# Kernel optimization log

Measured on AMD Instinct MI355X. Metric: run time of the kernel, lower is better.

## Reference

```python
import jax, jax.numpy as jnp
import numpy as np

B, D_IMG, D_NUM, P = 16384, 2048, 256, 128

def setup_inputs() -> dict:
    key = jax.random.key(0)
    ks = jax.random.split(key, 12)
    s = lambda d: 1.0 / np.sqrt(d)
    return {
        "img_feat": jax.random.normal(ks[0], (B, D_IMG), jnp.float32),
        "num_feat": jax.random.normal(ks[1], (B, D_NUM), jnp.float32),
        "Wi1": jax.random.uniform(ks[2], (D_IMG, P), jnp.float32, -s(D_IMG), s(D_IMG)),
        "bi1": jax.random.uniform(ks[3], (P,), jnp.float32, -s(D_IMG), s(D_IMG)),
        "Wi2": jax.random.uniform(ks[4], (P, P), jnp.float32, -s(P), s(P)),
        "bi2": jax.random.uniform(ks[5], (P,), jnp.float32, -s(P), s(P)),
        "Wn1": jax.random.uniform(ks[6], (D_NUM, P), jnp.float32, -s(D_NUM), s(D_NUM)),
        "bn1": jax.random.uniform(ks[7], (P,), jnp.float32, -s(D_NUM), s(D_NUM)),
        "Wn2": jax.random.uniform(ks[8], (P, P), jnp.float32, -s(P), s(P)),
        "bn2": jax.random.uniform(ks[9], (P,), jnp.float32, -s(P), s(P)),
        "log_temp": jnp.asarray(np.log(0.1), jnp.float32),
    }

def _mlp(x, W1, b1, W2, b2):
    h = jax.nn.relu(x @ W1 + b1)
    return h @ W2 + b2

def _l2norm(x, eps=1e-12):
    # matches F.normalize(dim=1): x / max(||x||, eps)
    n = jnp.sqrt(jnp.sum(x * x, axis=1, keepdims=True))
    return x / jnp.maximum(n, eps)

def reference(img_feat, num_feat, Wi1, bi1, Wi2, bi2, Wn1, bn1, Wn2, bn2, log_temp):
    temp = jnp.exp(log_temp)
    ip = _l2norm(_mlp(img_feat, Wi1, bi1, Wi2, bi2))  # [B, P]
    npj = _l2norm(_mlp(num_feat, Wn1, bn1, Wn2, bn2))  # [B, P]
    logits = (ip @ npj.T) / temp                        # [B, B]
    # symmetric cross-entropy with labels = arange(B): targets on the diagonal
    lse_rows = jax.nn.logsumexp(logits, axis=1)  # i2n
    lse_cols = jax.nn.logsumexp(logits, axis=0)  # n2i (logits.T rows)
    diag = jnp.diagonal(logits)
    loss_i2n = jnp.mean(lse_rows - diag)
    loss_n2i = jnp.mean(lse_cols - diag)
    return (loss_i2n + loss_n2i) * 0.5
```

## Files before the change

kernel.cpp:

```cpp
#include <hip/hip_runtime.h>
#include <hip/hip_bf16.h>

typedef __bf16 bf16_t;
typedef __bf16 bf16x8 __attribute__((ext_vector_type(8)));
typedef float f32x4 __attribute__((ext_vector_type(4)));

#define NB 16384
#define NSPLIT 16
#define CG (NB / NSPLIT)
#define BNT 64
#define NT (CG / BNT)

__device__ inline bf16x8 ld8(const bf16_t* p) { return *(const bf16x8*)p; }

__device__ inline void gload_lds16(const bf16_t* g, bf16_t* l) {
  __builtin_amdgcn_global_load_lds(
      (const __attribute__((address_space(1))) unsigned int*)g,
      (__attribute__((address_space(3))) unsigned int*)l, 16, 0, 0);
}

__global__ void prep(const float* __restrict__ Wi1, const float* __restrict__ Wn1,
                     const float* __restrict__ Wi2, const float* __restrict__ Wn2,
                     bf16_t* __restrict__ Wi1t, bf16_t* __restrict__ Wn1t,
                     bf16_t* __restrict__ Wi2t, bf16_t* __restrict__ Wn2t,
                     float* __restrict__ lossacc) {
  int b = blockIdx.x;
  if (b < 1280) {
    int idx = b * 256 + threadIdx.x;
    if (idx < 262144) { int k = idx >> 7, n = idx & 127;
      Wi1t[n * 2048 + (k ^ ((n & 7) << 3))] = (bf16_t)Wi1[idx]; return; }
    idx -= 262144;
    if (idx < 32768) { int k = idx >> 7, n = idx & 127;
      Wn1t[n * 256 + (k ^ ((n & 7) << 3))] = (bf16_t)Wn1[idx]; return; }
    idx -= 32768;
    if (idx < 16384) { int k = idx >> 7, n = idx & 127;
      Wi2t[n * 128 + (k ^ ((n & 7) << 3))] = (bf16_t)Wi2[idx]; return; }
    idx -= 16384;
    { int k = idx >> 7, n = idx & 127;
      Wn2t[n * 128 + (k ^ ((n & 7) << 3))] = (bf16_t)Wn2[idx]; }
  } else {
    if (threadIdx.x < 2) lossacc[threadIdx.x] = 0.f;
  }
}

__global__ __launch_bounds__(256, 2) void mlp_fused(
    const float* __restrict__ imgf, const float* __restrict__ numf,
    const bf16_t* __restrict__ Wi1t, const bf16_t* __restrict__ Wn1t,
    const bf16_t* __restrict__ Wi2t, const bf16_t* __restrict__ Wn2t,
    const float* __restrict__ bi1, const float* __restrict__ bn1,
    const float* __restrict__ bi2, const float* __restrict__ bn2,
    bf16_t* __restrict__ ipb, bf16_t* __restrict__ npb) {
  __shared__ bf16_t As[2][32 * 128];
  __shared__ bf16_t Bs[2][128 * 128];
  const int bid = blockIdx.x;
  const bool isnum = bid >= 512;
  const float*  Xf = isnum ? numf : imgf;
  const bf16_t* W1 = isnum ? Wn1t : Wi1t;
  const bf16_t* W2 = isnum ? Wn2t : Wi2t;
  const float* b1  = isnum ? bn1 : bi1;
  const float* b2  = isnum ? bn2 : bi2;
  bf16_t* Out = isnum ? npb : ipb;
  const int K = isnum ? 256 : 2048;
  const int NK = K >> 7;
  const int t = threadIdx.x, l = t & 63, wid = t >> 6;
  const int wm = wid >> 1, wn = wid & 1;
  const int row0 = (bid & 511) * 32;

  auto stageA = [&](int kk, int buf) {
#pragma unroll
    for (int i = 0; i < 2; i++) {
      int s = t + i * 256;
      int r = s >> 4, c = s & 15;
      const float* src = Xf + (size_t)(row0 + r) * K + kk * 128 + c * 8;
      float4 f0 = *(const float4*)(src);
      float4 f1 = *(const float4*)(src + 4);
      bf16x8 v;
      v[0]=(bf16_t)f0.x; v[1]=(bf16_t)f0.y; v[2]=(bf16_t)f0.z; v[3]=(bf16_t)f0.w;
      v[4]=(bf16_t)f1.x; v[5]=(bf16_t)f1.y; v[6]=(bf16_t)f1.z; v[7]=(bf16_t)f1.w;
      *(bf16x8*)(As[buf] + r * 128 + ((c ^ (r & 7)) << 3)) = v;
    }
  };
  auto stageB = [&](int kk, int buf) {
#pragma unroll
    for (int i = 0; i < 8; i++) {
      int s = t + i * 256;
      gload_lds16(W1 + (size_t)(s >> 4) * K + kk * 128 + (s & 15) * 8,
                  Bs[buf] + s * 8);
    }
  };

  f32x4 acc[4];
#pragma unroll
  for (int j = 0; j < 4; j++) acc[j] = (f32x4){0.f, 0.f, 0.f, 0.f};

  stageA(0, 0);
  stageB(0, 0);
  __syncthreads();

  for (int kk = 0; kk < NK; kk++) {
    const int cur = kk & 1;
    if (kk + 1 < NK) {
      stageA(kk + 1, cur ^ 1);
      stageB(kk + 1, cur ^ 1);
    }
#pragma unroll
    for (int ks = 0; ks < 4; ks++) {
      int r = wm * 16 + (l & 15);
      int c = ks * 4 + (l >> 4);
      bf16x8 a = ld8(As[cur] + r * 128 + ((c ^ (r & 7)) << 3));
#pragma unroll
      for (int nt = 0; nt < 4; nt++) {
        int rb = wn * 64 + nt * 16 + (l & 15);
        bf16x8 bfr = ld8(Bs[cur] + rb * 128 + ((c ^ (rb & 7)) << 3));
        acc[nt] = __builtin_amdgcn_mfma_f32_16x16x32_bf16(a, bfr, acc[nt], 0, 0, 0);
      }
    }
    __syncthreads();
  }

  float* rnorm = (float*)As[1];
#pragma unroll
  for (int i = 0; i < 8; i++) {
    int s = t + i * 256;
    gload_lds16(W2 + (size_t)(s >> 4) * 128 + (s & 15) * 8, Bs[0] + s * 8);
  }
  if (t < 32) rnorm[t] = 0.f;
  {
    int rbase = wm * 16 + ((l >> 4) << 2);
#pragma unroll
    for (int nt = 0; nt < 4; nt++) {
      int col = wn * 64 + nt * 16 + (l & 15);
      float bv = b1[col];
#pragma unroll
      for (int r4 = 0; r4 < 4; r4++) {
        int row = rbase + r4;
        float h = fmaxf(acc[nt][r4] + bv, 0.f);
        As[0][row * 128 + (col ^ ((row & 7) << 3))] = (bf16_t)h;
      }
    }
  }
  __syncthreads();

  f32x4 acc2[4];
#pragma unroll
  for (int j = 0; j < 4; j++) acc2[j] = (f32x4){0.f, 0.f, 0.f, 0.f};
#pragma unroll
  for (int ks = 0; ks < 4; ks++) {
    int r = wm * 16 + (l & 15);
    int c = ks * 4 + (l >> 4);
    bf16x8 a = ld8(As[0] + r * 128 + ((c ^ (r & 7)) << 3));
#pragma unroll
    for (int nt = 0; nt < 4; nt++) {
      int rb = wn * 64 + nt * 16 + (l & 15);
      bf16x8 bfr = ld8(Bs[0] + rb * 128 + ((c ^ (rb & 7)) << 3));
      acc2[nt] = __builtin_amdgcn_mfma_f32_16x16x32_bf16(a, bfr, acc2[nt], 0, 0, 0);
    }
  }
  float vv[4][4];
#pragma unroll
  for (int nt = 0; nt < 4; nt++) {
    int col = wn * 64 + nt * 16 + (l & 15);
    float bv = b2[col];
#pragma unroll
    for (int r4 = 0; r4 < 4; r4++) vv[nt][r4] = acc2[nt][r4] + bv;
  }
#pragma unroll
  for (int r4 = 0; r4 < 4; r4++) {
    float p = 0.f;
#pragma unroll
    for (int nt = 0; nt < 4; nt++) p += vv[nt][r4] * vv[nt][r4];
    p += __shfl_xor(p, 1); p += __shfl_xor(p, 2);
    p += __shfl_xor(p, 4); p += __shfl_xor(p, 8);
    if ((l & 15) == 0) atomicAdd(&rnorm[wm * 16 + ((l >> 4) << 2) + r4], p);
  }
  __syncthreads();
#pragma unroll
  for (int r4 = 0; r4 < 4; r4++) {
    int rl = wm * 16 + ((l >> 4) << 2) + r4;
    float sc = 1.f / fmaxf(sqrtf(rnorm[rl]), 1e-12f);
#pragma unroll
    for (int nt = 0; nt < 4; nt++) {
      int col = wn * 64 + nt * 16 + (l & 15);
      int swcol = col ^ ((rl & 7) << 3);
      Out[(size_t)(row0 + rl) * 128 + swcol] = (bf16_t)(vv[nt][r4] * sc);
    }
  }
}

__global__ __launch_bounds__(512, 4) void logits_split(
    const bf16_t* __restrict__ IP, const bf16_t* __restrict__ NP,
    const float* __restrict__ log_temp, float* __restrict__ rowpart,
    float* __restrict__ colpart, float* __restrict__ diag) {
  __shared__ bf16_t BsAll[2 * BNT * 128];
  __shared__ float colred[CG];
  __shared__ float rowred[2][128];
  int bid = blockIdx.x;
  int sw = (bid & 7) * (128 * NSPLIT / 8) + (bid >> 3);
  int bm = sw >> 4, g = sw & (NSPLIT - 1);
  const int t = threadIdx.x, l = t & 63, wid = t >> 6;
  const int wm = wid >> 1, wn = wid & 1;
  const float invt = __expf(-log_temp[0]);
  const float kk = invt * 1.44269504088896f;

  for (int i = t; i < CG; i += 512) colred[i] = 0.f;
#pragma unroll
  for (int i = 0; i < 4; i++) {
    int s = t + i * 512;
    gload_lds16(IP + (size_t)bm * (128 * 128) + s * 8, BsAll + s * 8);
  }
  __syncthreads();
  bf16x8 af[2][4];
#pragma unroll
  for (int mt = 0; mt < 2; mt++) {
    int r = wm * 32 + mt * 16 + (l & 15);
#pragma unroll
    for (int ks = 0; ks < 4; ks++) {
      int c = ks * 4 + (l >> 4);
      af[mt][ks] = ld8(BsAll + r * 128 + ((c ^ (r & 7)) << 3));
    }
  }
  __syncthreads();
#pragma unroll
  for (int i = 0; i < 2; i++) {
    int s = t + i * 512;
    gload_lds16(NP + (size_t)(g * CG) * 128 + s * 8, BsAll + s * 8);
  }
  __syncthreads();

  f32x4 racc[2];
  racc[0] = (f32x4){0.f, 0.f, 0.f, 0.f};
  racc[1] = (f32x4){0.f, 0.f, 0.f, 0.f};

#pragma unroll 1
  for (int tl = 0; tl < NT; tl++) {
    bf16_t* Bsc = BsAll + (tl & 1) * (BNT * 128);
    if (tl + 1 < NT) {
      bf16_t* Bsn = BsAll + ((tl + 1) & 1) * (BNT * 128);
      const bf16_t* src = NP + (size_t)(g * CG + (tl + 1) * BNT) * 128;
#pragma unroll
      for (int i = 0; i < 2; i++) {
        int s = t + i * 512;
        gload_lds16(src + s * 8, Bsn + s * 8);
      }
    }
    f32x4 acc[2][2];
#pragma unroll
    for (int i = 0; i < 2; i++)
#pragma unroll
      for (int j = 0; j < 2; j++) acc[i][j] = (f32x4){0.f, 0.f, 0.f, 0.f};
#pragma unroll
    for (int ks = 0; ks < 4; ks++) {
      int c = ks * 4 + (l >> 4);
      bf16x8 b[2];
#pragma unroll
      for (int nt = 0; nt < 2; nt++) {
        int rb = wn * 32 + nt * 16 + (l & 15);
        b[nt] = ld8(Bsc + rb * 128 + ((c ^ (rb & 7)) << 3));
      }
#pragma unroll
      for (int mt = 0; mt < 2; mt++) {
        acc[mt][0] = __builtin_amdgcn_mfma_f32_16x16x32_bf16(af[mt][ks], b[0], acc[mt][0], 0, 0, 0);
        acc[mt][1] = __builtin_amdgcn_mfma_f32_16x16x32_bf16(af[mt][ks], b[1], acc[mt][1], 0, 0, 0);
      }
    }
    const int colbase = g * CG + tl * BNT;
    if ((colbase >> 7) == bm) {
#pragma unroll
      for (int mt = 0; mt < 2; mt++)
#pragma unroll
        for (int nt = 0; nt < 2; nt++)
#pragma unroll
          for (int r4 = 0; r4 < 4; r4++) {
            int gr = bm * 128 + wm * 32 + mt * 16 + ((l >> 4) << 2) + r4;
            int gc = colbase + wn * 32 + nt * 16 + (l & 15);
            if (gr == gc) diag[gr] = acc[mt][nt][r4] * invt;
          }
    }
#pragma unroll
    for (int mt = 0; mt < 2; mt++)
#pragma unroll
      for (int nt = 0; nt < 2; nt++) {
        f32x4 y = acc[mt][nt] * kk - kk;
#pragma unroll
        for (int r4 = 0; r4 < 4; r4++) acc[mt][nt][r4] = __builtin_amdgcn_exp2f(y[r4]);
      }
#pragma unroll
    for (int mt = 0; mt < 2; mt++) racc[mt] += acc[mt][0] + acc[mt][1];
#pragma unroll
    for (int nt = 0; nt < 2; nt++) {
      f32x4 cv = acc[0][nt] + acc[1][nt];
      float cs = (cv[0] + cv[1]) + (cv[2] + cv[3]);
      cs += __shfl_xor(cs, 16); cs += __shfl_xor(cs, 32);
      if (l < 16) atomicAdd(&colred[tl * BNT + wn * 32 + nt * 16 + l], cs);
    }
    __syncthreads();
  }
#pragma unroll
  for (int mt = 0; mt < 2; mt++)
#pragma unroll
    for (int r4 = 0; r4 < 4; r4++) {
      float rs = racc[mt][r4];
      rs += __shfl_xor(rs, 1); rs += __shfl_xor(rs, 2);
      rs += __shfl_xor(rs, 4); rs += __shfl_xor(rs, 8);
      if ((l & 15) == 0)
        rowred[wn][wm * 32 + mt * 16 + ((l >> 4) << 2) + r4] = rs;
    }
  __syncthreads();
  if (t < 128)
    rowpart[(size_t)g * NB + bm * 128 + t] = rowred[0][t] + rowred[1][t];
  for (int c = t; c < CG; c += 512)
    colpart[(size_t)bm * NB + g * CG + c] = colred[c];
}

__global__ void finalize(const float* __restrict__ rowpart, const float* __restrict__ colpart,
                         const float* __restrict__ diag, const float* __restrict__ log_temp,
                         float* __restrict__ lossacc, float* __restrict__ out) {
  int i = blockIdx.x * 64 + threadIdx.x;
  float rsum = 0.f, csum = 0.f;
#pragma unroll
  for (int g = 0; g < NSPLIT; g++) rsum += rowpart[(size_t)g * NB + i];
#pragma unroll 16
  for (int b = 0; b < 128; b++) csum += colpart[(size_t)b * NB + i];
  float v = 0.5f * (logf(rsum) + logf(csum)) - diag[i];
  for (int m = 1; m < 64; m <<= 1) v += __shfl_xor(v, m);
  if (threadIdx.x == 0) {
    atomicAdd(lossacc, v);
    __threadfence();
    unsigned n = atomicAdd((unsigned*)(lossacc + 1), 1u);
    if (n == gridDim.x - 1) {
      float tot = atomicAdd(lossacc, 0.f);
      out[0] = tot / (float)NB + __expf(-log_temp[0]);
    }
  }
}

extern "C" void kernel_launch(void* const* d_in, const int* in_sizes, int n_in,
                              void* d_out, int out_size, void* d_ws, size_t ws_size,
                              hipStream_t stream) {
  const float* img = (const float*)d_in[0];
  const float* num = (const float*)d_in[1];
  const float* Wi1 = (const float*)d_in[2];
  const float* bi1 = (const float*)d_in[3];
  const float* Wi2 = (const float*)d_in[4];
  const float* bi2 = (const float*)d_in[5];
  const float* Wn1 = (const float*)d_in[6];
  const float* bn1 = (const float*)d_in[7];
  const float* Wn2 = (const float*)d_in[8];
  const float* bn2 = (const float*)d_in[9];
  const float* log_temp = (const float*)d_in[10];
  float* out = (float*)d_out;

  char* w = (char*)d_ws;
  bf16_t* ipb  = (bf16_t*)(w);
  bf16_t* npb  = (bf16_t*)(w + (4u << 20));
  float* colpart = (float*)(w + (8u << 20));
  bf16_t* Wi1t = (bf16_t*)(w + (16u << 20));
  bf16_t* Wn1t = (bf16_t*)(w + (16u << 20) + (512u << 10));
  bf16_t* Wi2t = (bf16_t*)(w + (16u << 20) + (576u << 10));
  bf16_t* Wn2t = (bf16_t*)(w + (16u << 20) + (640u << 10));
  float* rowpart = (float*)(w + (16u << 20));
  float* diag    = (float*)(w + (17u << 20));
  float* lossacc = (float*)(w + (17u << 20) + (64u << 10));

  prep<<<dim3(1281), 256, 0, stream>>>(Wi1, Wn1, Wi2, Wn2,
                                       Wi1t, Wn1t, Wi2t, Wn2t, lossacc);
  mlp_fused<<<dim3(1024), 256, 0, stream>>>(img, num, Wi1t, Wn1t, Wi2t, Wn2t,
                                            bi1, bn1, bi2, bn2, ipb, npb);
  logits_split<<<dim3(128 * NSPLIT), 512, 0, stream>>>(ipb, npb, log_temp,
                                                       rowpart, colpart, diag);
  finalize<<<dim3(NB / 64), 64, 0, stream>>>(rowpart, colpart, diag, log_temp,
                                             lossacc, out);
}
```

Measured before the change: 356.5 us.

## Split MLP launch per path, enlarge logits warp tiles, split finalize reduction

The fused MLP kernel is split into two launches, one for the image path and one for the numeric path, so each branch is specialized and K is passed in. The logits kernel moves from 512 to 256 threads per block, so each warp computes 64 rows instead of 32 and reuses every loaded B fragment across four MFMA row tiles, at the cost of more registers and an occupancy bound of 3. The finalize step is split into a wide column-sum kernel and a separate loss kernel to parallelize the 128-way column reduction better. This adds one extra launch and an intermediate buffer.

```diff
diff --git a/kernel.cpp b/kernel.cpp
--- a/kernel.cpp
+++ b/kernel.cpp
@@ -43,28 +43,16 @@
   }
 }
 
-__global__ __launch_bounds__(256, 2) void mlp_fused(
-    const float* __restrict__ imgf, const float* __restrict__ numf,
-    const bf16_t* __restrict__ Wi1t, const bf16_t* __restrict__ Wn1t,
-    const bf16_t* __restrict__ Wi2t, const bf16_t* __restrict__ Wn2t,
-    const float* __restrict__ bi1, const float* __restrict__ bn1,
-    const float* __restrict__ bi2, const float* __restrict__ bn2,
-    bf16_t* __restrict__ ipb, bf16_t* __restrict__ npb) {
+__global__ __launch_bounds__(256, 2) void mlp_path(
+    const float* __restrict__ Xf, const bf16_t* __restrict__ W1,
+    const bf16_t* __restrict__ W2, const float* __restrict__ b1,
+    const float* __restrict__ b2, bf16_t* __restrict__ Out, int K) {
   __shared__ bf16_t As[2][32 * 128];
   __shared__ bf16_t Bs[2][128 * 128];
-  const int bid = blockIdx.x;
-  const bool isnum = bid >= 512;
-  const float*  Xf = isnum ? numf : imgf;
-  const bf16_t* W1 = isnum ? Wn1t : Wi1t;
-  const bf16_t* W2 = isnum ? Wn2t : Wi2t;
-  const float* b1  = isnum ? bn1 : bi1;
-  const float* b2  = isnum ? bn2 : bi2;
-  bf16_t* Out = isnum ? npb : ipb;
-  const int K = isnum ? 256 : 2048;
   const int NK = K >> 7;
   const int t = threadIdx.x, l = t & 63, wid = t >> 6;
   const int wm = wid >> 1, wn = wid & 1;
-  const int row0 = (bid & 511) * 32;
+  const int row0 = blockIdx.x * 32;
 
   auto stageA = [&](int kk, int buf) {
 #pragma unroll
@@ -187,7 +175,7 @@
   }
 }
 
-__global__ __launch_bounds__(512, 4) void logits_split(
+__global__ __launch_bounds__(256, 3) void logits_split(
     const bf16_t* __restrict__ IP, const bf16_t* __restrict__ NP,
     const float* __restrict__ log_temp, float* __restrict__ rowpart,
     float* __restrict__ colpart, float* __restrict__ diag) {
@@ -202,17 +190,17 @@
   const float invt = __expf(-log_temp[0]);
   const float kk = invt * 1.44269504088896f;
 
-  for (int i = t; i < CG; i += 512) colred[i] = 0.f;
-#pragma unroll
-  for (int i = 0; i < 4; i++) {
-    int s = t + i * 512;
+  for (int i = t; i < CG; i += 256) colred[i] = 0.f;
+#pragma unroll
+  for (int i = 0; i < 8; i++) {
+    int s = t + i * 256;
     gload_lds16(IP + (size_t)bm * (128 * 128) + s * 8, BsAll + s * 8);
   }
   __syncthreads();
-  bf16x8 af[2][4];
-#pragma unroll
-  for (int mt = 0; mt < 2; mt++) {
-    int r = wm * 32 + mt * 16 + (l & 15);
+  bf16x8 af[4][4];
+#pragma unroll
+  for (int mt = 0; mt < 4; mt++) {
+    int r = wm * 64 + mt * 16 + (l & 15);
 #pragma unroll
     for (int ks = 0; ks < 4; ks++) {
       int c = ks * 4 + (l >> 4);
@@ -221,15 +209,15 @@
   }
   __syncthreads();
 #pragma unroll
-  for (int i = 0; i < 2; i++) {
-    int s = t + i * 512;
+  for (int i = 0; i < 4; i++) {
+    int s = t + i * 256;
     gload_lds16(NP + (size_t)(g * CG) * 128 + s * 8, BsAll + s * 8);
   }
   __syncthreads();
 
-  f32x4 racc[2];
-  racc[0] = (f32x4){0.f, 0.f, 0.f, 0.f};
-  racc[1] = (f32x4){0.f, 0.f, 0.f, 0.f};
+  f32x4 racc[4];
+#pragma unroll
+  for (int a = 0; a < 4; a++) racc[a] = (f32x4){0.f, 0.f, 0.f, 0.f};
 
 #pragma unroll 1
   for (int tl = 0; tl < NT; tl++) {
@@ -238,14 +226,14 @@
       bf16_t* Bsn = BsAll + ((tl + 1) & 1) * (BNT * 128);
       const bf16_t* src = NP + (size_t)(g * CG + (tl + 1) * BNT) * 128;
 #pragma unroll
-      for (int i = 0; i < 2; i++) {
-        int s = t + i * 512;
+      for (int i = 0; i < 4; i++) {
+        int s = t + i * 256;
         gload_lds16(src + s * 8, Bsn + s * 8);
       }
     }
-    f32x4 acc[2][2];
-#pragma unroll
-    for (int i = 0; i < 2; i++)
+    f32x4 acc[4][2];
+#pragma unroll
+    for (int i = 0; i < 4; i++)
 #pragma unroll
       for (int j = 0; j < 2; j++) acc[i][j] = (f32x4){0.f, 0.f, 0.f, 0.f};
 #pragma unroll
@@ -258,7 +246,7 @@
         b[nt] = ld8(Bsc + rb * 128 + ((c ^ (rb & 7)) << 3));
       }
 #pragma unroll
-      for (int mt = 0; mt < 2; mt++) {
+      for (int mt = 0; mt < 4; mt++) {
         acc[mt][0] = __builtin_amdgcn_mfma_f32_16x16x32_bf16(af[mt][ks], b[0], acc[mt][0], 0, 0, 0);
         acc[mt][1] = __builtin_amdgcn_mfma_f32_16x16x32_bf16(af[mt][ks], b[1], acc[mt][1], 0, 0, 0);
       }
@@ -266,18 +254,18 @@
     const int colbase = g * CG + tl * BNT;
     if ((colbase >> 7) == bm) {
 #pragma unroll
-      for (int mt = 0; mt < 2; mt++)
+      for (int mt = 0; mt < 4; mt++)
 #pragma unroll
         for (int nt = 0; nt < 2; nt++)
 #pragma unroll
           for (int r4 = 0; r4 < 4; r4++) {
-            int gr = bm * 128 + wm * 32 + mt * 16 + ((l >> 4) << 2) + r4;
+            int gr = bm * 128 + wm * 64 + mt * 16 + ((l >> 4) << 2) + r4;
             int gc = colbase + wn * 32 + nt * 16 + (l & 15);
             if (gr == gc) diag[gr] = acc[mt][nt][r4] * invt;
           }
     }
 #pragma unroll
-    for (int mt = 0; mt < 2; mt++)
+    for (int mt = 0; mt < 4; mt++)
 #pragma unroll
       for (int nt = 0; nt < 2; nt++) {
         f32x4 y = acc[mt][nt] * kk - kk;
@@ -285,10 +273,10 @@
         for (int r4 = 0; r4 < 4; r4++) acc[mt][nt][r4] = __builtin_amdgcn_exp2f(y[r4]);
       }
 #pragma unroll
-    for (int mt = 0; mt < 2; mt++) racc[mt] += acc[mt][0] + acc[mt][1];
+    for (int mt = 0; mt < 4; mt++) racc[mt] += acc[mt][0] + acc[mt][1];
 #pragma unroll
     for (int nt = 0; nt < 2; nt++) {
-      f32x4 cv = acc[0][nt] + acc[1][nt];
+      f32x4 cv = (acc[0][nt] + acc[1][nt]) + (acc[2][nt] + acc[3][nt]);
       float cs = (cv[0] + cv[1]) + (cv[2] + cv[3]);
       cs += __shfl_xor(cs, 16); cs += __shfl_xor(cs, 32);
       if (l < 16) atomicAdd(&colred[tl * BNT + wn * 32 + nt * 16 + l], cs);
@@ -296,32 +284,38 @@
     __syncthreads();
   }
 #pragma unroll
-  for (int mt = 0; mt < 2; mt++)
+  for (int mt = 0; mt < 4; mt++)
 #pragma unroll
     for (int r4 = 0; r4 < 4; r4++) {
       float rs = racc[mt][r4];
       rs += __shfl_xor(rs, 1); rs += __shfl_xor(rs, 2);
       rs += __shfl_xor(rs, 4); rs += __shfl_xor(rs, 8);
       if ((l & 15) == 0)
-        rowred[wn][wm * 32 + mt * 16 + ((l >> 4) << 2) + r4] = rs;
+        rowred[wn][wm * 64 + mt * 16 + ((l >> 4) << 2) + r4] = rs;
     }
   __syncthreads();
   if (t < 128)
     rowpart[(size_t)g * NB + bm * 128 + t] = rowred[0][t] + rowred[1][t];
-  for (int c = t; c < CG; c += 512)
+  for (int c = t; c < CG; c += 256)
     colpart[(size_t)bm * NB + g * CG + c] = colred[c];
 }
 
-__global__ void finalize(const float* __restrict__ rowpart, const float* __restrict__ colpart,
-                         const float* __restrict__ diag, const float* __restrict__ log_temp,
-                         float* __restrict__ lossacc, float* __restrict__ out) {
+__global__ void colsum_k(const float* __restrict__ colpart, float* __restrict__ colsum) {
+  int i = blockIdx.x * 256 + threadIdx.x;
+  float s = 0.f;
+#pragma unroll 16
+  for (int b = 0; b < 128; b++) s += colpart[(size_t)b * NB + i];
+  colsum[i] = s;
+}
+
+__global__ void loss_k(const float* __restrict__ rowpart, const float* __restrict__ colsum,
+                       const float* __restrict__ diag, const float* __restrict__ log_temp,
+                       float* __restrict__ lossacc, float* __restrict__ out) {
   int i = blockIdx.x * 64 + threadIdx.x;
-  float rsum = 0.f, csum = 0.f;
+  float rsum = 0.f;
 #pragma unroll
   for (int g = 0; g < NSPLIT; g++) rsum += rowpart[(size_t)g * NB + i];
-#pragma unroll 16
-  for (int b = 0; b < 128; b++) csum += colpart[(size_t)b * NB + i];
-  float v = 0.5f * (logf(rsum) + logf(csum)) - diag[i];
+  float v = 0.5f * (logf(rsum) + logf(colsum[i])) - diag[i];
   for (int m = 1; m < 64; m <<= 1) v += __shfl_xor(v, m);
   if (threadIdx.x == 0) {
     atomicAdd(lossacc, v);
@@ -360,14 +354,16 @@
   bf16_t* Wn2t = (bf16_t*)(w + (16u << 20) + (640u << 10));
   float* rowpart = (float*)(w + (16u << 20));
   float* diag    = (float*)(w + (17u << 20));
-  float* lossacc = (float*)(w + (17u << 20) + (64u << 10));
+  float* colsum  = (float*)(w + (17u << 20) + (64u << 10));
+  float* lossacc = (float*)(w + (17u << 20) + (128u << 10));
 
   prep<<<dim3(1281), 256, 0, stream>>>(Wi1, Wn1, Wi2, Wn2,
                                        Wi1t, Wn1t, Wi2t, Wn2t, lossacc);
-  mlp_fused<<<dim3(1024), 256, 0, stream>>>(img, num, Wi1t, Wn1t, Wi2t, Wn2t,
-                                            bi1, bn1, bi2, bn2, ipb, npb);
-  logits_split<<<dim3(128 * NSPLIT), 512, 0, stream>>>(ipb, npb, log_temp,
+  mlp_path<<<dim3(512), 256, 0, stream>>>(img, Wi1t, Wi2t, bi1, bi2, ipb, 2048);
+  mlp_path<<<dim3(512), 256, 0, stream>>>(num, Wn1t, Wn2t, bn1, bn2, npb, 256);
+  logits_split<<<dim3(128 * NSPLIT), 256, 0, stream>>>(ipb, npb, log_temp,
                                                        rowpart, colpart, diag);
-  finalize<<<dim3(NB / 64), 64, 0, stream>>>(rowpart, colpart, diag, log_temp,
-                                             lossacc, out);
-}
+  colsum_k<<<dim3(NB / 256), 256, 0, stream>>>(colpart, colsum);
+  loss_k<<<dim3(NB / 64), 64, 0, stream>>>(rowpart, colsum, diag, log_temp,
+                                           lossacc, out);
+}
```

After: 337.9 us. 1.06x faster.
